# Kernel tuning notes

Hardware: AMD Instinct MI355X
Metric: run time of the kernel (lower is better)

The kernel has to match this reference:

```python
import jax, jax.numpy as jnp
import numpy as np

B = 8388608  # batch size


def _ry(angle):
    """RY(angle) 2x2 real rotation; angle shape [...] -> [..., 2, 2]."""
    c = jnp.cos(angle * 0.5)
    s = jnp.sin(angle * 0.5)
    row0 = jnp.stack([c, -s], axis=-1)
    row1 = jnp.stack([s, c], axis=-1)
    return jnp.stack([row0, row1], axis=-2)


def setup_inputs() -> dict:
    key = jax.random.key(0)
    k1, k2 = jax.random.split(key)
    features = jax.random.normal(k1, (B, 2), dtype=jnp.float32)
    theta = jax.random.normal(k2, (2, 2), dtype=jnp.float32) * 0.1
    return {"features": features, "theta": theta}


def reference(features, theta):
    # 2-qubit real state, shape [B, 2, 2]: axis 1 = wire0, axis 2 = wire1.
    # All gates (RY, CNOT) are real, so no complex arithmetic needed.
    b = features.shape[0]
    state = jnp.zeros((b, 2, 2), dtype=features.dtype).at[:, 0, 0].set(1.0)

    # Data-encoding rotations: RY(x1) on wire0, RY(x2) on wire1 (per-sample angles)
    u0 = _ry(features[:, 0])  # [B,2,2]
    u1 = _ry(features[:, 1])  # [B,2,2]
    state = jnp.einsum('bik,bkj->bij', u0, state)
    state = jnp.einsum('bjk,bik->bij', u1, state)

    # Two variational layers: RY(theta[l,0]) w0, RY(theta[l,1]) w1, CNOT(0,1)
    for layer in range(2):
        ua = _ry(theta[layer, 0])  # [2,2]
        ub = _ry(theta[layer, 1])  # [2,2]
        state = jnp.einsum('ik,bkj->bij', ua, state)
        state = jnp.einsum('jk,bik->bij', ub, state)
        # CNOT(control=0, target=1): flip wire1 where wire0 == 1
        state = jnp.stack([state[:, 0, :], state[:, 1, ::-1]], axis=1)

    # <Z0> = P(wire0=0) - P(wire0=1)
    z0 = jnp.sum(state[:, 0, :] ** 2 - state[:, 1, :] ** 2, axis=-1)
    return z0[:, None]  # [B, 1]
```

## Files before the change

kernel.cpp:

```cpp
#include <hip/hip_runtime.h>


__global__ __launch_bounds__(256) void tqc_kernel(
    const float4* __restrict__ feat,
    const float*  __restrict__ theta,
    float4*       __restrict__ out,
    int n4)
{
    int t = blockIdx.x * blockDim.x + threadIdx.x;
    if (t >= n4) return;

    float ca0, sa0, cb0, sb0, ca1, sa1, cb1, sb1;
    __sincosf(0.5f * theta[0], &sa0, &ca0);
    __sincosf(0.5f * theta[1], &sb0, &cb0);
    __sincosf(0.5f * theta[2], &sa1, &ca1);
    __sincosf(0.5f * theta[3], &sb1, &cb1);

    float4 f0 = feat[2 * t];
    float4 f1 = feat[2 * t + 1];
    float xs[8] = {f0.x, f0.y, f0.z, f0.w, f1.x, f1.y, f1.z, f1.w};

    float res[4];
#pragma unroll
    for (int k = 0; k < 4; ++k) {
        float c0, s0, c1, s1;
        __sincosf(0.5f * xs[2 * k],     &s0, &c0);
        __sincosf(0.5f * xs[2 * k + 1], &s1, &c1);
        float a = c0 * c1;
        float b = c0 * s1;
        float c = s0 * c1;
        float d = s0 * s1;

        float na = ca0 * a - sa0 * c, nb = ca0 * b - sa0 * d;
        float nc = sa0 * a + ca0 * c, nd = sa0 * b + ca0 * d;
        a = cb0 * na - sb0 * nb;
        b = sb0 * na + cb0 * nb;
        float c2 = cb0 * nc - sb0 * nd;
        float d2 = sb0 * nc + cb0 * nd;
        c = d2;
        d = c2;

        na = ca1 * a - sa1 * c; nb = ca1 * b - sa1 * d;
        nc = sa1 * a + ca1 * c; nd = sa1 * b + ca1 * d;
        a = cb1 * na - sb1 * nb;
        b = sb1 * na + cb1 * nb;
        c2 = cb1 * nc - sb1 * nd;
        d2 = sb1 * nc + cb1 * nd;
        c = d2;
        d = c2;

        res[k] = a * a + b * b - c * c - d * d;
    }

    out[t] = make_float4(res[0], res[1], res[2], res[3]);
}

extern "C" void kernel_launch(void* const* d_in, const int* in_sizes, int n_in,
                              void* d_out, int out_size, void* d_ws, size_t ws_size,
                              hipStream_t stream) {
    const float* feat  = (const float*)d_in[0];
    const float* theta = (const float*)d_in[1];
    float* out = (float*)d_out;

    int b  = in_sizes[0] / 2;
    int n4 = b / 4;
    int block = 256;
    int grid = (n4 + block - 1) / block;
    tqc_kernel<<<grid, block, 0, stream>>>(
        (const float4*)feat, theta, (float4*)out, n4);
}
```

Before: 97.30 us.

## Precompute theta circuit as quadratic form and evaluate per sample with full-angle trig

Collapses the fixed variational layers and the Z0 measurement into a 3x3 coefficient matrix over (1, cos x, sin x) terms, computed once by a single-thread setup kernel into workspace. The main kernel then evaluates each sample with two sincos calls and a small bilinear form instead of the full gate sequence. Each thread now handles two samples instead of four. This adds a serial tiny kernel launch and a dependency on workspace, in exchange for far less per-sample arithmetic.

```diff
diff --git a/kernel.cpp b/kernel.cpp
--- a/kernel.cpp
+++ b/kernel.cpp
@@ -1,58 +1,91 @@
 #include <hip/hip_runtime.h>
 
 
-__global__ __launch_bounds__(256) void tqc_kernel(
-    const float4* __restrict__ feat,
-    const float*  __restrict__ theta,
-    float4*       __restrict__ out,
-    int n4)
+__global__ void tqc_setup(const float* __restrict__ theta, float* __restrict__ W) {
+    float ang[4] = {theta[0], theta[1], theta[2], theta[3]};
+
+    float M[4][4], K[4][4], T2[4][4];
+    for (int i = 0; i < 4; ++i)
+        for (int j = 0; j < 4; ++j) M[i][j] = (i == j) ? 1.f : 0.f;
+
+    for (int l = 0; l < 2; ++l) {
+        float ca = cosf(0.5f * ang[2 * l]),     sa = sinf(0.5f * ang[2 * l]);
+        float cb = cosf(0.5f * ang[2 * l + 1]), sb = sinf(0.5f * ang[2 * l + 1]);
+        float A[2][2]  = {{ca, -sa}, {sa, ca}};
+        float Bb[2][2] = {{cb, -sb}, {sb, cb}};
+        for (int i = 0; i < 2; ++i)
+            for (int j = 0; j < 2; ++j)
+                for (int k = 0; k < 2; ++k)
+                    for (int m = 0; m < 2; ++m)
+                        K[2 * i + j][2 * k + m] = A[i][k] * Bb[j][m];
+        for (int i = 0; i < 4; ++i)
+            for (int j = 0; j < 4; ++j) {
+                float acc = 0.f;
+                for (int k = 0; k < 4; ++k) acc += K[i][k] * M[k][j];
+                T2[i][j] = acc;
+            }
+        for (int j = 0; j < 4; ++j) {
+            M[0][j] = T2[0][j];
+            M[1][j] = T2[1][j];
+            M[2][j] = T2[3][j];
+            M[3][j] = T2[2][j];
+        }
+    }
+
+    float Q[4][4];
+    for (int r = 0; r < 4; ++r)
+        for (int c = 0; c < 4; ++c) {
+            float acc = 0.f;
+            for (int t = 0; t < 4; ++t) {
+                float d = (t < 2) ? 1.f : -1.f;
+                acc += M[t][r] * d * M[t][c];
+            }
+            Q[r][c] = acc;
+        }
+
+    const float T[2][2][3] = {{{0.5f, 0.5f, 0.f}, {0.f, 0.f, 0.5f}},
+                              {{0.f, 0.f, 0.5f}, {0.5f, -0.5f, 0.f}}};
+    for (int m = 0; m < 3; ++m)
+        for (int n = 0; n < 3; ++n) {
+            float acc = 0.f;
+            for (int a = 0; a < 2; ++a)
+                for (int b = 0; b < 2; ++b)
+                    for (int c = 0; c < 2; ++c)
+                        for (int d = 0; d < 2; ++d)
+                            acc += Q[2 * a + b][2 * c + d] * T[a][c][m] * T[b][d][n];
+            W[3 * m + n] = acc;
+        }
+}
+
+__global__ __launch_bounds__(256) void tqc_main(
+    const float4* __restrict__ feat4,
+    const float*  __restrict__ W,
+    float2*       __restrict__ out2,
+    int n2)
 {
     int t = blockIdx.x * blockDim.x + threadIdx.x;
-    if (t >= n4) return;
+    if (t >= n2) return;
 
-    float ca0, sa0, cb0, sb0, ca1, sa1, cb1, sb1;
-    __sincosf(0.5f * theta[0], &sa0, &ca0);
-    __sincosf(0.5f * theta[1], &sb0, &cb0);
-    __sincosf(0.5f * theta[2], &sa1, &ca1);
-    __sincosf(0.5f * theta[3], &sb1, &cb1);
+    float w0 = W[0], w1 = W[1], w2 = W[2];
+    float w3 = W[3], w4 = W[4], w5 = W[5];
+    float w6 = W[6], w7 = W[7], w8 = W[8];
 
-    float4 f0 = feat[2 * t];
-    float4 f1 = feat[2 * t + 1];
-    float xs[8] = {f0.x, f0.y, f0.z, f0.w, f1.x, f1.y, f1.z, f1.w};
+    float4 f = feat4[t];
 
-    float res[4];
-#pragma unroll
-    for (int k = 0; k < 4; ++k) {
-        float c0, s0, c1, s1;
-        __sincosf(0.5f * xs[2 * k],     &s0, &c0);
-        __sincosf(0.5f * xs[2 * k + 1], &s1, &c1);
-        float a = c0 * c1;
-        float b = c0 * s1;
-        float c = s0 * c1;
-        float d = s0 * s1;
+    float s1, c1, s2, c2;
+    __sincosf(f.x, &s1, &c1);
+    __sincosf(f.y, &s2, &c2);
+    float r0 = (w0 + w1 * c2 + w2 * s2)
+             + c1 * (w3 + w4 * c2 + w5 * s2)
+             + s1 * (w6 + w7 * c2 + w8 * s2);
 
-        float na = ca0 * a - sa0 * c, nb = ca0 * b - sa0 * d;
-        float nc = sa0 * a + ca0 * c, nd = sa0 * b + ca0 * d;
-        a = cb0 * na - sb0 * nb;
-        b = sb0 * na + cb0 * nb;
-        float c2 = cb0 * nc - sb0 * nd;
-        float d2 = sb0 * nc + cb0 * nd;
-        c = d2;
-        d = c2;
+    __sincosf(f.z, &s1, &c1);
+    __sincosf(f.w, &s2, &c2);
+    float r1 = (w0 + w1 * c2 + w2 * s2)
+             + c1 * (w3 + w4 * c2 + w5 * s2)
+             + s1 * (w6 + w7 * c2 + w8 * s2);
 
-        na = ca1 * a - sa1 * c; nb = ca1 * b - sa1 * d;
-        nc = sa1 * a + ca1 * c; nd = sa1 * b + ca1 * d;
-        a = cb1 * na - sb1 * nb;
-        b = sb1 * na + cb1 * nb;
-        c2 = cb1 * nc - sb1 * nd;
-        d2 = sb1 * nc + cb1 * nd;
-        c = d2;
-        d = c2;
-
-        res[k] = a * a + b * b - c * c - d * d;
-    }
-
-    out[t] = make_float4(res[0], res[1], res[2], res[3]);
+    out2[t] = make_float2(r0, r1);
 }
 
 extern "C" void kernel_launch(void* const* d_in, const int* in_sizes, int n_in,
@@ -61,11 +94,15 @@
     const float* feat  = (const float*)d_in[0];
     const float* theta = (const float*)d_in[1];
     float* out = (float*)d_out;
+    float* W   = (float*)d_ws;
 
     int b  = in_sizes[0] / 2;
-    int n4 = b / 4;
+    int n2 = b / 2;
+
+    tqc_setup<<<1, 1, 0, stream>>>(theta, W);
+
     int block = 256;
-    int grid = (n4 + block - 1) / block;
-    tqc_kernel<<<grid, block, 0, stream>>>(
-        (const float4*)feat, theta, (float4*)out, n4);
+    int grid = (n2 + block - 1) / block;
+    tqc_main<<<grid, block, 0, stream>>>(
+        (const float4*)feat, W, (float2*)out, n2);
 }
```

Result: slower. 100.8 us (+3.6%).

## Replace per-sample gate simulation with closed-form expectation value

Applied to the files above, without the earlier changes.

Derives <Z0> analytically as cos(A)cos(x1+B) - sin(A)sin(x1+B)sin(x2+C). This drops the 2x2 gate chain and cuts the transcendental calls per sample from two sincos to one sincos plus one sin. The final wire-1 rotation and the last CNOT drop out because they do not change <Z0>. Each thread now reads one float4 from each half of the batch and writes float2 outputs to matching halves, which changes the access pattern but keeps accesses coalesced.

```diff
diff --git a/kernel.cpp b/kernel.cpp
--- a/kernel.cpp
+++ b/kernel.cpp
@@ -1,58 +1,44 @@
 #include <hip/hip_runtime.h>
 
 
-__global__ __launch_bounds__(256) void tqc_kernel(
-    const float4* __restrict__ feat,
+__global__ __launch_bounds__(256) void tqc_closed(
+    const float4* __restrict__ feat4,
     const float*  __restrict__ theta,
-    float4*       __restrict__ out,
-    int n4)
+    float2*       __restrict__ out2,
+    int half)
 {
     int t = blockIdx.x * blockDim.x + threadIdx.x;
-    if (t >= n4) return;
+    if (t >= half) return;
 
-    float ca0, sa0, cb0, sb0, ca1, sa1, cb1, sb1;
-    __sincosf(0.5f * theta[0], &sa0, &ca0);
-    __sincosf(0.5f * theta[1], &sb0, &cb0);
-    __sincosf(0.5f * theta[2], &sa1, &ca1);
-    __sincosf(0.5f * theta[3], &sb1, &cb1);
+    float Bc = theta[0];
+    float Cc = theta[1];
+    float sA, cA;
+    __sincosf(theta[2], &sA, &cA);
 
-    float4 f0 = feat[2 * t];
-    float4 f1 = feat[2 * t + 1];
-    float xs[8] = {f0.x, f0.y, f0.z, f0.w, f1.x, f1.y, f1.z, f1.w};
+    float4 f0 = feat4[t];
+    float4 f1 = feat4[t + half];
 
-    float res[4];
-#pragma unroll
-    for (int k = 0; k < 4; ++k) {
-        float c0, s0, c1, s1;
-        __sincosf(0.5f * xs[2 * k],     &s0, &c0);
-        __sincosf(0.5f * xs[2 * k + 1], &s1, &c1);
-        float a = c0 * c1;
-        float b = c0 * s1;
-        float c = s0 * c1;
-        float d = s0 * s1;
+    float s1, c1, s2;
 
-        float na = ca0 * a - sa0 * c, nb = ca0 * b - sa0 * d;
-        float nc = sa0 * a + ca0 * c, nd = sa0 * b + ca0 * d;
-        a = cb0 * na - sb0 * nb;
-        b = sb0 * na + cb0 * nb;
-        float c2 = cb0 * nc - sb0 * nd;
-        float d2 = sb0 * nc + cb0 * nd;
-        c = d2;
-        d = c2;
+    __sincosf(f0.x + Bc, &s1, &c1);
+    s2 = __sinf(f0.y + Cc);
+    float r0 = cA * c1 - sA * s1 * s2;
 
-        na = ca1 * a - sa1 * c; nb = ca1 * b - sa1 * d;
-        nc = sa1 * a + ca1 * c; nd = sa1 * b + ca1 * d;
-        a = cb1 * na - sb1 * nb;
-        b = sb1 * na + cb1 * nb;
-        c2 = cb1 * nc - sb1 * nd;
-        d2 = sb1 * nc + cb1 * nd;
-        c = d2;
-        d = c2;
+    __sincosf(f0.z + Bc, &s1, &c1);
+    s2 = __sinf(f0.w + Cc);
+    float r1 = cA * c1 - sA * s1 * s2;
 
-        res[k] = a * a + b * b - c * c - d * d;
-    }
+    out2[t] = make_float2(r0, r1);
 
-    out[t] = make_float4(res[0], res[1], res[2], res[3]);
+    __sincosf(f1.x + Bc, &s1, &c1);
+    s2 = __sinf(f1.y + Cc);
+    r0 = cA * c1 - sA * s1 * s2;
+
+    __sincosf(f1.z + Bc, &s1, &c1);
+    s2 = __sinf(f1.w + Cc);
+    r1 = cA * c1 - sA * s1 * s2;
+
+    out2[t + half] = make_float2(r0, r1);
 }
 
 extern "C" void kernel_launch(void* const* d_in, const int* in_sizes, int n_in,
@@ -62,10 +48,12 @@
     const float* theta = (const float*)d_in[1];
     float* out = (float*)d_out;
 
-    int b  = in_sizes[0] / 2;
-    int n4 = b / 4;
+    int b    = in_sizes[0] / 2;
+    int n4   = b / 2;
+    int half = n4 / 2;
+
     int block = 256;
-    int grid = (n4 + block - 1) / block;
-    tqc_kernel<<<grid, block, 0, stream>>>(
-        (const float4*)feat, theta, (float4*)out, n4);
+    int grid = (half + block - 1) / block;
+    tqc_closed<<<grid, block, 0, stream>>>(
+        (const float4*)feat, theta, (float2*)out, half);
 }
```

Result: no change. 96.31 us (median of 2 runs) (-1.0%).
